# Kernel tuning notes

Measured on AMD Instinct MI355X. Metric: run time of the kernel, lower is better.

## Reference

```python
import jax, jax.numpy as jnp
import numpy as np
from jax import lax

VOCAB, EMBED, HID, B, T = 100, 50, 30, 512, 512
PAD_ID = 0


def setup_inputs() -> dict:
    key = jax.random.key(0)
    ks = jax.random.split(key, 16)
    s_e = 1.0 / np.sqrt(HID)  # torch LSTM/Linear uniform(-1/sqrt(H), 1/sqrt(H)) style
    def u(k, shape, s):
        return jax.random.uniform(k, shape, jnp.float32, -s, s)
    batch_x = jax.random.randint(ks[0], (B, T), 0, VOCAB)
    lens = jax.random.randint(ks[1], (B,), 1, T + 1)
    lens = lens.at[0].set(T)  # ensure pad_packed max length == T
    embedding = jax.random.normal(ks[2], (VOCAB, EMBED), jnp.float32)
    embedding = embedding.at[PAD_ID].set(0.0)  # padding_idx row
    return {
        "batch_x": batch_x,
        "batch_x_lens": lens,
        "embedding": embedding,
        "w_ih1": u(ks[3], (4 * HID, EMBED), s_e),
        "w_hh1": u(ks[4], (4 * HID, HID), s_e),
        "b_ih1": u(ks[5], (4 * HID,), s_e),
        "b_hh1": u(ks[6], (4 * HID,), s_e),
        "w_ih2": u(ks[7], (4 * HID, HID), s_e),
        "w_hh2": u(ks[8], (4 * HID, HID), s_e),
        "b_ih2": u(ks[9], (4 * HID,), s_e),
        "b_hh2": u(ks[10], (4 * HID,), s_e),
        "lw1": u(ks[11], (HID, HID), s_e),
        "lb1": u(ks[12], (HID,), s_e),
        "lw2": u(ks[13], (VOCAB, HID), s_e),
        "lb2": u(ks[14], (VOCAB,), s_e),
    }


def _lstm(x_tbe, mask_tb, w_ih, w_hh, b_ih, b_hh):
    """Masked LSTM over time; state frozen where mask==0 (packed-sequence semantics).
    x_tbe: [T,B,E]; mask_tb: [T,B] bool. Returns hidden seq [T,B,H]."""
    H = w_hh.shape[1]
    Bn = x_tbe.shape[1]
    # precompute input projections for all timesteps (one big GEMM)
    xp = jnp.einsum("tbe,ge->tbg", x_tbe, w_ih) + b_ih + b_hh  # [T,B,4H]

    def step(carry, inp):
        h, c = carry
        xt, mt = inp
        gates = xt + h @ w_hh.T
        i, f, g, o = jnp.split(gates, 4, axis=-1)  # torch gate order i,f,g,o
        i = jax.nn.sigmoid(i)
        f = jax.nn.sigmoid(f)
        g = jnp.tanh(g)
        o = jax.nn.sigmoid(o)
        c_new = f * c + i * g
        h_new = o * jnp.tanh(c_new)
        m = mt[:, None]
        h = jnp.where(m, h_new, h)
        c = jnp.where(m, c_new, c)
        return (h, c), h

    init = (jnp.zeros((Bn, H), x_tbe.dtype), jnp.zeros((Bn, H), x_tbe.dtype))
    _, hs = lax.scan(step, init, (xp, mask_tb))
    return hs


def reference(batch_x, batch_x_lens, embedding,
              w_ih1, w_hh1, b_ih1, b_hh1,
              w_ih2, w_hh2, b_ih2, b_hh2,
              lw1, lb1, lw2, lb2):
    Bn, Tn = batch_x.shape
    mask = (jnp.arange(Tn)[None, :] < batch_x_lens[:, None])  # [B,T]
    x = embedding[batch_x]                                     # [B,T,E]
    x = jnp.transpose(x, (1, 0, 2))                            # [T,B,E]
    m_tb = mask.T                                              # [T,B]
    h1 = _lstm(x, m_tb, w_ih1, w_hh1, b_ih1, b_hh1)            # [T,B,H]
    h2 = _lstm(h1, m_tb, w_ih2, w_hh2, b_ih2, b_hh2)           # [T,B,H]
    out = jnp.transpose(h2, (1, 0, 2))                         # [B,T,H]
    out = jnp.where(mask[:, :, None], out, 0.0)                # pad_packed zero-fill
    hmid = jax.nn.relu(out @ lw1.T + lb1)
    return hmid @ lw2.T + lb2                                  # [B,T,vocab]
```

## Files before the change

kernel.cpp:

```cpp
#include <hip/hip_runtime.h>
#include <math.h>

#define VOCABN 100
#define EMBEDN 50
#define HID 30
#define NB 512
#define NT 512
#define G4 120
#define S 16
#define RD 32

#define L2E 1.44269504089f
#define L2E2 2.88539008178f

__device__ __forceinline__ float fastrcp(float x) {
  float r;
  asm("v_rcp_f32 %0, %1" : "=v"(r) : "v"(x));
  return r;
}
__device__ __forceinline__ float fexp2(float x) {
  float r;
  asm("v_exp_f32 %0, %1" : "=v"(r) : "v"(x));
  return r;
}
__device__ __forceinline__ void bcast_halves(float x, float& lo_all, float& hi_all) {
  auto r = __builtin_amdgcn_permlane32_swap(__builtin_bit_cast(unsigned, x),
                                            __builtin_bit_cast(unsigned, x), false, false);
  lo_all = __builtin_bit_cast(float, (unsigned)r[0]);
  hi_all = __builtin_bit_cast(float, (unsigned)r[1]);
}
__device__ __forceinline__ float rdlane(float v, int k) {
  return __builtin_bit_cast(float, __builtin_amdgcn_readlane(__builtin_bit_cast(int, v), k));
}
__device__ __forceinline__ void tick_barrier() {
  asm volatile("s_waitcnt lgkmcnt(0)" ::: "memory");
  __builtin_amdgcn_s_barrier();
  asm volatile("" ::: "memory");
}

__global__ void prep_kernel(const float* __restrict__ emb,
                            const float* __restrict__ w_ih1,
                            const float* __restrict__ b_ih1,
                            const float* __restrict__ b_hh1,
                            const float* __restrict__ b_ih2,
                            const float* __restrict__ b_hh2,
                            const float* __restrict__ lw2,
                            const float* __restrict__ lb1,
                            const float* __restrict__ lb2,
                            float* __restrict__ xpe, float* __restrict__ b2s,
                            float* __restrict__ outc) {
  __shared__ float e[EMBEDN];
  int r = blockIdx.x;
  int tid = threadIdx.x;
  if (tid < EMBEDN) e[tid] = emb[r * EMBEDN + tid];
  __syncthreads();
  if (tid < G4) {
    float s = b_ih1[tid] + b_hh1[tid];
#pragma unroll
    for (int k = 0; k < EMBEDN; ++k) s = fmaf(e[k], w_ih1[tid * EMBEDN + k], s);
    float sc = (tid >= 2 * HID && tid < 3 * HID) ? L2E2 : L2E;
    xpe[r * G4 + tid] = s * sc;
    if (r == 0) b2s[tid] = (b_ih2[tid] + b_hh2[tid]) * sc;
  }
  if (r == 0 && tid < VOCABN) {
    float o = lb2[tid];
#pragma unroll
    for (int k = 0; k < HID; ++k) o = fmaf(fmaxf(lb1[k], 0.f), lw2[tid * HID + k], o);
    outc[tid] = o;
  }
}

__global__ void __launch_bounds__(256) scan_kernel(
    const int* __restrict__ batch_x, const int* __restrict__ lens,
    const float* __restrict__ xpe, const float* __restrict__ b2s,
    const float* __restrict__ w_hh1, const float* __restrict__ w_ih2,
    const float* __restrict__ w_hh2,
    const float* __restrict__ lw1, const float* __restrict__ lb1,
    const float* __restrict__ lw2, const float* __restrict__ lb2,
    const float* __restrict__ outc, float* __restrict__ out) {
  __shared__ __align__(16) float h1ring[RD][32];
  __shared__ __align__(16) float2 uring[RD][64];
  __shared__ __align__(16) float h2ring[RD][32];
  __shared__ int tok_lds[NT];

  const int b = blockIdx.x;
  const int tid = threadIdx.x;
  const int wid = tid >> 6;
  const int lane = tid & 63;
  const int half = lane >> 5;
  const int j = lane & 31;
  const int jj = (j < HID) ? j : (HID - 1);
  const int gA = half ? (jj + 2 * HID) : jj;
  const int gB = gA + HID;

  const int* xrow = batch_x + b * NT;
  for (int i = tid; i < NT; i += 256) tok_lds[i] = xrow[i];

  const int len = lens[b];
  const int K = (len + S - 1) / S;
  __syncthreads();

  if (wid < 3) {
    const float C1 = half ? 1.0f : L2E2;
    const float C2 = half ? 2.0f : L2E2;
    const float scA = half ? L2E2 : L2E;
    const float* wsrc = (wid == 0) ? w_hh1 : (wid == 1) ? w_ih2 : w_hh2;
    float wA[HID], wB[HID];
#pragma unroll
    for (int k = 0; k < HID; ++k) {
      wA[k] = wsrc[gA * HID + k] * scA;
      wB[k] = wsrc[gB * HID + k] * L2E;
    }
    const float b2A = b2s[gA], b2B = b2s[gB];

    if (wid == 0) {
      float cs1 = 0.f;
      float hs1[HID];
#pragma unroll
      for (int k = 0; k < HID; ++k) hs1[k] = 0.f;
      int tk = tok_lds[0];
      float xa0 = xpe[tk * G4 + gA], xb0 = xpe[tk * G4 + gB];
      tk = tok_lds[1];
      float xa1 = xpe[tk * G4 + gA], xb1 = xpe[tk * G4 + gB];
      tk = tok_lds[2];
      float xa2 = xpe[tk * G4 + gA], xb2 = xpe[tk * G4 + gB];
      int t = 0;
      for (int k = 0; k < K + 3; ++k) {
        if (k < K) {
          int tend = (k + 1) * S;
          tend = (tend < len) ? tend : len;
          for (; t < tend; ++t) {
            float a0a = 0.f, a0b = 0.f, a1a = 0.f, a1b = 0.f;
#pragma unroll
            for (int p = 0; p < 15; ++p) {
              a0a = fmaf(hs1[p], wA[p], a0a);
              a1a = fmaf(hs1[p], wB[p], a1a);
              a0b = fmaf(hs1[p + 15], wA[p + 15], a0b);
              a1b = fmaf(hs1[p + 15], wB[p + 15], a1b);
            }
            float a0 = a0a + a0b + xa0;
            float a1 = a1a + a1b + xb0;
            float sA = C1 - C2 * fastrcp(1.0f + fexp2(a0));
            float sB = 1.0f - fastrcp(1.0f + fexp2(a1));
            float iL, g1, f1, o1;
            bcast_halves(sA, iL, g1);
            bcast_halves(sB, f1, o1);
            cs1 = fmaf(f1, cs1, iL * g1);
            float rr = fastrcp(1.0f + fexp2(cs1));
            float h1n = fmaf(-2.0f * o1, rr, o1);
            if (lane < 32) h1ring[t & (RD - 1)][j] = h1n;
#pragma unroll
            for (int q = 0; q < HID; ++q) hs1[q] = rdlane(h1n, q);
            xa0 = xa1; xb0 = xb1;
            xa1 = xa2; xb1 = xb2;
            int tn = t + 3;
            tk = tok_lds[(tn < NT) ? tn : (NT - 1)];
            xa2 = xpe[tk * G4 + gA];
            xb2 = xpe[tk * G4 + gB];
          }
        }
        tick_barrier();
      }
    } else if (wid == 1) {
      int t = 0;
      for (int k = 0; k < K + 3; ++k) {
        if (k >= 1 && k <= K) {
          int tend = k * S;
          tend = (tend < len) ? tend : len;
          for (; t < tend; ++t) {
            const float2* hp = (const float2*)h1ring[t & (RD - 1)];
            float2 hv[15];
#pragma unroll
            for (int p = 0; p < 15; ++p) hv[p] = hp[p];
            float q0a = 0.f, q0b = 0.f, q1a = 0.f, q1b = 0.f;
#pragma unroll
            for (int p = 0; p < 15; ++p) {
              if (p < 8) {
                q0a = fmaf(hv[p].x, wA[2 * p], q0a);
                q1a = fmaf(hv[p].x, wB[2 * p], q1a);
                q0a = fmaf(hv[p].y, wA[2 * p + 1], q0a);
                q1a = fmaf(hv[p].y, wB[2 * p + 1], q1a);
              } else {
                q0b = fmaf(hv[p].x, wA[2 * p], q0b);
                q1b = fmaf(hv[p].x, wB[2 * p], q1b);
                q0b = fmaf(hv[p].y, wA[2 * p + 1], q0b);
                q1b = fmaf(hv[p].y, wB[2 * p + 1], q1b);
              }
            }
            float2 u;
            u.x = q0a + q0b;
            u.y = q1a + q1b;
            uring[t & (RD - 1)][lane] = u;
          }
        }
        tick_barrier();
      }
    } else {
      float cs2 = 0.f;
      float hs2[HID];
#pragma unroll
      for (int k = 0; k < HID; ++k) hs2[k] = 0.f;
      int t = 0;
      for (int k = 0; k < K + 3; ++k) {
        if (k >= 2) {
          int tend = (k - 1) * S;
          tend = (tend < len) ? tend : len;
          for (; t < tend; ++t) {
            float2 u = uring[t & (RD - 1)][lane];
            float q0a = 0.f, q0b = 0.f, q1a = 0.f, q1b = 0.f;
#pragma unroll
            for (int p = 0; p < 15; ++p) {
              q0a = fmaf(hs2[p], wA[p], q0a);
              q1a = fmaf(hs2[p], wB[p], q1a);
              q0b = fmaf(hs2[p + 15], wA[p + 15], q0b);
              q1b = fmaf(hs2[p + 15], wB[p + 15], q1b);
            }
            float q0 = q0a + q0b + u.x + b2A;
            float q1 = q1a + q1b + u.y + b2B;
            float sA = C1 - C2 * fastrcp(1.0f + fexp2(q0));
            float sB = 1.0f - fastrcp(1.0f + fexp2(q1));
            float iL, g2, f2, o2;
            bcast_halves(sA, iL, g2);
            bcast_halves(sB, f2, o2);
            cs2 = fmaf(f2, cs2, iL * g2);
            float rr = fastrcp(1.0f + fexp2(cs2));
            float h2n = fmaf(-2.0f * o2, rr, o2);
            if (lane < 32) h2ring[t & (RD - 1)][j] = h2n;
#pragma unroll
            for (int q = 0; q < HID; ++q) hs2[q] = rdlane(h2n, q);
          }
        }
        tick_barrier();
      }
    }
  } else {
    const int l1 = (lane < 50) ? lane : 49;
    float w1x[15], w1y[15];
#pragma unroll
    for (int p = 0; p < 15; ++p) {
      w1x[p] = lw1[jj * HID + 2 * p];
      w1y[p] = lw1[jj * HID + 2 * p + 1];
    }
    float w2a[HID], w2b[HID];
#pragma unroll
    for (int k = 0; k < HID; ++k) {
      w2a[k] = lw2[l1 * HID + k];
      w2b[k] = lw2[(l1 + 50) * HID + k];
    }
    const float lb1v = lb1[jj];
    const float lb2a = lb2[l1], lb2b = lb2[l1 + 50];
    const float oca = outc[l1], ocb = outc[l1 + 50];

    int t = 0;
    for (int k = 0; k < K + 3; ++k) {
      if (k >= 3) {
        int tend = (k - 2) * S;
        tend = (tend < len) ? tend : len;
        for (; t < tend; ++t) {
          const float2* hp = (const float2*)h2ring[t & (RD - 1)];
          float2 h[15];
#pragma unroll
          for (int p = 0; p < 15; ++p) h[p] = hp[p];
          float ma = lb1v, mb = 0.f;
#pragma unroll
          for (int p = 0; p < 15; ++p) {
            if (p < 8) {
              ma = fmaf(h[p].x, w1x[p], ma);
              ma = fmaf(h[p].y, w1y[p], ma);
            } else {
              mb = fmaf(h[p].x, w1x[p], mb);
              mb = fmaf(h[p].y, w1y[p], mb);
            }
          }
          float m = fmaxf(ma + mb, 0.f);
          float sm[HID];
#pragma unroll
          for (int q = 0; q < HID; ++q) sm[q] = rdlane(m, q);
          float oa0 = lb2a, oa1 = 0.f, ob0 = lb2b, ob1 = 0.f;
#pragma unroll
          for (int q = 0; q < 15; ++q) {
            oa0 = fmaf(sm[q], w2a[q], oa0);
            ob0 = fmaf(sm[q], w2b[q], ob0);
            oa1 = fmaf(sm[q + 15], w2a[q + 15], oa1);
            ob1 = fmaf(sm[q + 15], w2b[q + 15], ob1);
          }
          float* orow = out + ((size_t)(b * NT + t)) * VOCABN;
          if (lane < 50) {
            orow[l1] = oa0 + oa1;
            orow[l1 + 50] = ob0 + ob1;
          }
        }
      }
      tick_barrier();
    }
    for (int tt = len; tt < NT; ++tt) {
      float* orow = out + ((size_t)(b * NT + tt)) * VOCABN;
      if (lane < 50) {
        orow[l1] = oca;
        orow[l1 + 50] = ocb;
      }
    }
  }
}

extern "C" void kernel_launch(void* const* d_in, const int* in_sizes, int n_in,
                              void* d_out, int out_size, void* d_ws, size_t ws_size,
                              hipStream_t stream) {
  const int* batch_x = (const int*)d_in[0];
  const int* lens = (const int*)d_in[1];
  const float* emb = (const float*)d_in[2];
  const float* w_ih1 = (const float*)d_in[3];
  const float* w_hh1 = (const float*)d_in[4];
  const float* b_ih1 = (const float*)d_in[5];
  const float* b_hh1 = (const float*)d_in[6];
  const float* w_ih2 = (const float*)d_in[7];
  const float* w_hh2 = (const float*)d_in[8];
  const float* b_ih2 = (const float*)d_in[9];
  const float* b_hh2 = (const float*)d_in[10];
  const float* lw1 = (const float*)d_in[11];
  const float* lb1 = (const float*)d_in[12];
  const float* lw2 = (const float*)d_in[13];
  const float* lb2 = (const float*)d_in[14];
  float* out = (float*)d_out;

  char* ws = (char*)d_ws;
  float* xpe = (float*)ws;
  float* b2s = (float*)(ws + 48 * 1024);
  float* outc = (float*)(ws + 56 * 1024);

  prep_kernel<<<VOCABN, 128, 0, stream>>>(emb, w_ih1, b_ih1, b_hh1, b_ih2, b_hh2,
                                          lw2, lb1, lb2, xpe, b2s, outc);
  scan_kernel<<<NB, 256, 0, stream>>>(batch_x, lens, xpe, b2s, w_hh1, w_ih2, w_hh2,
                                      lw1, lb1, lw2, lb2, outc, out);
}
```

Before: 268.9 us.

## Use packed fp16 dot2 for recurrent matvecs and compute all four gates per lane

The recurrent h@W_hh products in both LSTM layers now use fp16-packed weights and hidden state with v_dot2 accumulation into fp32. Each lane computes all four gates for its hidden unit, so the permlane32 half-swap broadcast is no longer needed. The change targets the latency of the serial per-timestep critical path by halving the FMA count and removing the cross-half exchange. In exchange it adds fp16 rounding (round-toward-zero) to weights and hidden state, which can cause accuracy drift over 512 recurrent steps, and it shortens the input-projection prefetch depth from three steps to two.

```diff
diff --git a/kernel.cpp b/kernel.cpp
--- a/kernel.cpp
+++ b/kernel.cpp
@@ -13,6 +13,8 @@
 #define L2E 1.44269504089f
 #define L2E2 2.88539008178f
 
+typedef __fp16 h2v __attribute__((ext_vector_type(2)));
+
 __device__ __forceinline__ float fastrcp(float x) {
   float r;
   asm("v_rcp_f32 %0, %1" : "=v"(r) : "v"(x));
@@ -22,12 +24,6 @@
   float r;
   asm("v_exp_f32 %0, %1" : "=v"(r) : "v"(x));
   return r;
-}
-__device__ __forceinline__ void bcast_halves(float x, float& lo_all, float& hi_all) {
-  auto r = __builtin_amdgcn_permlane32_swap(__builtin_bit_cast(unsigned, x),
-                                            __builtin_bit_cast(unsigned, x), false, false);
-  lo_all = __builtin_bit_cast(float, (unsigned)r[0]);
-  hi_all = __builtin_bit_cast(float, (unsigned)r[1]);
 }
 __device__ __forceinline__ float rdlane(float v, int k) {
   return __builtin_bit_cast(float, __builtin_amdgcn_readlane(__builtin_bit_cast(int, v), k));
@@ -70,6 +66,32 @@
   }
 }
 
+#define DOT4(ai, af, ag, ao, HP, W0_, W1_, W2_, W3_, I0, I1, I2, I3)  \
+  float ai = (I0), af = (I1), ag = (I2), ao = (I3);                   \
+  float ai1 = 0.f, af1 = 0.f, ag1 = 0.f, ao1 = 0.f;                   \
+  _Pragma("unroll") for (int p = 0; p < 8; ++p) {                     \
+    ai = __builtin_amdgcn_fdot2(HP[p], W0_[p], ai, false);            \
+    af = __builtin_amdgcn_fdot2(HP[p], W1_[p], af, false);            \
+    ag = __builtin_amdgcn_fdot2(HP[p], W2_[p], ag, false);            \
+    ao = __builtin_amdgcn_fdot2(HP[p], W3_[p], ao, false);            \
+  }                                                                   \
+  _Pragma("unroll") for (int p = 8; p < 15; ++p) {                    \
+    ai1 = __builtin_amdgcn_fdot2(HP[p], W0_[p], ai1, false);          \
+    af1 = __builtin_amdgcn_fdot2(HP[p], W1_[p], af1, false);          \
+    ag1 = __builtin_amdgcn_fdot2(HP[p], W2_[p], ag1, false);          \
+    ao1 = __builtin_amdgcn_fdot2(HP[p], W3_[p], ao1, false);          \
+  }                                                                   \
+  ai += ai1; af += af1; ag += ag1; ao += ao1;
+
+#define NONLIN_H(ai, af, ag, ao, cs, hout)                 \
+  float iS = L2E2 - L2E2 * fastrcp(1.0f + fexp2(ai));      \
+  float f_ = 1.0f - fastrcp(1.0f + fexp2(af));             \
+  float g_ = 1.0f - 2.0f * fastrcp(1.0f + fexp2(ag));      \
+  float o_ = 1.0f - fastrcp(1.0f + fexp2(ao));             \
+  cs = fmaf(f_, cs, iS * g_);                              \
+  float rr = fastrcp(1.0f + fexp2(cs));                    \
+  float hout = fmaf(-2.0f * o_, rr, o_);
+
 __global__ void __launch_bounds__(256) scan_kernel(
     const int* __restrict__ batch_x, const int* __restrict__ lens,
     const float* __restrict__ xpe, const float* __restrict__ b2s,
@@ -90,8 +112,6 @@
   const int half = lane >> 5;
   const int j = lane & 31;
   const int jj = (j < HID) ? j : (HID - 1);
-  const int gA = half ? (jj + 2 * HID) : jj;
-  const int gB = gA + HID;
 
   const int* xrow = batch_x + b * NT;
   for (int i = tid; i < NT; i += 256) tok_lds[i] = xrow[i];
@@ -100,138 +120,122 @@
   const int K = (len + S - 1) / S;
   __syncthreads();
 
-  if (wid < 3) {
-    const float C1 = half ? 1.0f : L2E2;
-    const float C2 = half ? 2.0f : L2E2;
-    const float scA = half ? L2E2 : L2E;
-    const float* wsrc = (wid == 0) ? w_hh1 : (wid == 1) ? w_ih2 : w_hh2;
-    float wA[HID], wB[HID];
-#pragma unroll
-    for (int k = 0; k < HID; ++k) {
-      wA[k] = wsrc[gA * HID + k] * scA;
-      wB[k] = wsrc[gB * HID + k] * L2E;
-    }
-    const float b2A = b2s[gA], b2B = b2s[gB];
+  if (wid == 0 || wid == 2) {
+    const float* wsrc = (wid == 0) ? w_hh1 : w_hh2;
+    h2v wfi[15], wff[15], wfg[15], wfo[15];
+#pragma unroll
+    for (int p = 0; p < 15; ++p) {
+      const float* ri = wsrc + (0 * HID + jj) * HID;
+      const float* rf = wsrc + (1 * HID + jj) * HID;
+      const float* rg = wsrc + (2 * HID + jj) * HID;
+      const float* ro = wsrc + (3 * HID + jj) * HID;
+      wfi[p] = __builtin_amdgcn_cvt_pkrtz(ri[2 * p] * L2E, ri[2 * p + 1] * L2E);
+      wff[p] = __builtin_amdgcn_cvt_pkrtz(rf[2 * p] * L2E, rf[2 * p + 1] * L2E);
+      wfg[p] = __builtin_amdgcn_cvt_pkrtz(rg[2 * p] * L2E2, rg[2 * p + 1] * L2E2);
+      wfo[p] = __builtin_amdgcn_cvt_pkrtz(ro[2 * p] * L2E, ro[2 * p + 1] * L2E);
+    }
+    h2v hp[15];
+#pragma unroll
+    for (int p = 0; p < 15; ++p) hp[p] = h2v{(__fp16)0.0f, (__fp16)0.0f};
+    float cs = 0.f;
 
     if (wid == 0) {
-      float cs1 = 0.f;
-      float hs1[HID];
-#pragma unroll
-      for (int k = 0; k < HID; ++k) hs1[k] = 0.f;
       int tk = tok_lds[0];
-      float xa0 = xpe[tk * G4 + gA], xb0 = xpe[tk * G4 + gB];
+      float x0i = xpe[tk * G4 + jj], x0f = xpe[tk * G4 + HID + jj];
+      float x0g = xpe[tk * G4 + 2 * HID + jj], x0o = xpe[tk * G4 + 3 * HID + jj];
       tk = tok_lds[1];
-      float xa1 = xpe[tk * G4 + gA], xb1 = xpe[tk * G4 + gB];
-      tk = tok_lds[2];
-      float xa2 = xpe[tk * G4 + gA], xb2 = xpe[tk * G4 + gB];
+      float x1i = xpe[tk * G4 + jj], x1f = xpe[tk * G4 + HID + jj];
+      float x1g = xpe[tk * G4 + 2 * HID + jj], x1o = xpe[tk * G4 + 3 * HID + jj];
       int t = 0;
       for (int k = 0; k < K + 3; ++k) {
         if (k < K) {
           int tend = (k + 1) * S;
           tend = (tend < len) ? tend : len;
           for (; t < tend; ++t) {
-            float a0a = 0.f, a0b = 0.f, a1a = 0.f, a1b = 0.f;
-#pragma unroll
-            for (int p = 0; p < 15; ++p) {
-              a0a = fmaf(hs1[p], wA[p], a0a);
-              a1a = fmaf(hs1[p], wB[p], a1a);
-              a0b = fmaf(hs1[p + 15], wA[p + 15], a0b);
-              a1b = fmaf(hs1[p + 15], wB[p + 15], a1b);
-            }
-            float a0 = a0a + a0b + xa0;
-            float a1 = a1a + a1b + xb0;
-            float sA = C1 - C2 * fastrcp(1.0f + fexp2(a0));
-            float sB = 1.0f - fastrcp(1.0f + fexp2(a1));
-            float iL, g1, f1, o1;
-            bcast_halves(sA, iL, g1);
-            bcast_halves(sB, f1, o1);
-            cs1 = fmaf(f1, cs1, iL * g1);
-            float rr = fastrcp(1.0f + fexp2(cs1));
-            float h1n = fmaf(-2.0f * o1, rr, o1);
+            DOT4(ai, af, ag, ao, hp, wfi, wff, wfg, wfo, x0i, x0f, x0g, x0o)
+            NONLIN_H(ai, af, ag, ao, cs, h1n)
             if (lane < 32) h1ring[t & (RD - 1)][j] = h1n;
 #pragma unroll
-            for (int q = 0; q < HID; ++q) hs1[q] = rdlane(h1n, q);
-            xa0 = xa1; xb0 = xb1;
-            xa1 = xa2; xb1 = xb2;
-            int tn = t + 3;
+            for (int q = 0; q < 15; ++q)
+              hp[q] = __builtin_amdgcn_cvt_pkrtz(rdlane(h1n, 2 * q),
+                                                 rdlane(h1n, 2 * q + 1));
+            x0i = x1i; x0f = x1f; x0g = x1g; x0o = x1o;
+            int tn = t + 2;
             tk = tok_lds[(tn < NT) ? tn : (NT - 1)];
-            xa2 = xpe[tk * G4 + gA];
-            xb2 = xpe[tk * G4 + gB];
+            x1i = xpe[tk * G4 + jj];
+            x1f = xpe[tk * G4 + HID + jj];
+            x1g = xpe[tk * G4 + 2 * HID + jj];
+            x1o = xpe[tk * G4 + 3 * HID + jj];
           }
         }
         tick_barrier();
       }
-    } else if (wid == 1) {
-      int t = 0;
-      for (int k = 0; k < K + 3; ++k) {
-        if (k >= 1 && k <= K) {
-          int tend = k * S;
-          tend = (tend < len) ? tend : len;
-          for (; t < tend; ++t) {
-            const float2* hp = (const float2*)h1ring[t & (RD - 1)];
-            float2 hv[15];
-#pragma unroll
-            for (int p = 0; p < 15; ++p) hv[p] = hp[p];
-            float q0a = 0.f, q0b = 0.f, q1a = 0.f, q1b = 0.f;
-#pragma unroll
-            for (int p = 0; p < 15; ++p) {
-              if (p < 8) {
-                q0a = fmaf(hv[p].x, wA[2 * p], q0a);
-                q1a = fmaf(hv[p].x, wB[2 * p], q1a);
-                q0a = fmaf(hv[p].y, wA[2 * p + 1], q0a);
-                q1a = fmaf(hv[p].y, wB[2 * p + 1], q1a);
-              } else {
-                q0b = fmaf(hv[p].x, wA[2 * p], q0b);
-                q1b = fmaf(hv[p].x, wB[2 * p], q1b);
-                q0b = fmaf(hv[p].y, wA[2 * p + 1], q0b);
-                q1b = fmaf(hv[p].y, wB[2 * p + 1], q1b);
-              }
-            }
-            float2 u;
-            u.x = q0a + q0b;
-            u.y = q1a + q1b;
-            uring[t & (RD - 1)][lane] = u;
-          }
-        }
-        tick_barrier();
-      }
     } else {
-      float cs2 = 0.f;
-      float hs2[HID];
-#pragma unroll
-      for (int k = 0; k < HID; ++k) hs2[k] = 0.f;
+      const float b2i = b2s[jj], b2f = b2s[HID + jj];
+      const float b2g = b2s[2 * HID + jj], b2o = b2s[3 * HID + jj];
       int t = 0;
       for (int k = 0; k < K + 3; ++k) {
         if (k >= 2) {
           int tend = (k - 1) * S;
           tend = (tend < len) ? tend : len;
           for (; t < tend; ++t) {
-            float2 u = uring[t & (RD - 1)][lane];
-            float q0a = 0.f, q0b = 0.f, q1a = 0.f, q1b = 0.f;
-#pragma unroll
-            for (int p = 0; p < 15; ++p) {
-              q0a = fmaf(hs2[p], wA[p], q0a);
-              q1a = fmaf(hs2[p], wB[p], q1a);
-              q0b = fmaf(hs2[p + 15], wA[p + 15], q0b);
-              q1b = fmaf(hs2[p + 15], wB[p + 15], q1b);
-            }
-            float q0 = q0a + q0b + u.x + b2A;
-            float q1 = q1a + q1b + u.y + b2B;
-            float sA = C1 - C2 * fastrcp(1.0f + fexp2(q0));
-            float sB = 1.0f - fastrcp(1.0f + fexp2(q1));
-            float iL, g2, f2, o2;
-            bcast_halves(sA, iL, g2);
-            bcast_halves(sB, f2, o2);
-            cs2 = fmaf(f2, cs2, iL * g2);
-            float rr = fastrcp(1.0f + fexp2(cs2));
-            float h2n = fmaf(-2.0f * o2, rr, o2);
+            float2 uif = uring[t & (RD - 1)][jj];
+            float2 ugo = uring[t & (RD - 1)][jj + 32];
+            DOT4(ai, af, ag, ao, hp, wfi, wff, wfg, wfo,
+                 uif.x + b2i, uif.y + b2f, ugo.x + b2g, ugo.y + b2o)
+            NONLIN_H(ai, af, ag, ao, cs, h2n)
             if (lane < 32) h2ring[t & (RD - 1)][j] = h2n;
 #pragma unroll
-            for (int q = 0; q < HID; ++q) hs2[q] = rdlane(h2n, q);
+            for (int q = 0; q < 15; ++q)
+              hp[q] = __builtin_amdgcn_cvt_pkrtz(rdlane(h2n, 2 * q),
+                                                 rdlane(h2n, 2 * q + 1));
           }
         }
         tick_barrier();
       }
+    }
+  } else if (wid == 1) {
+    const int gA = half ? (jj + 2 * HID) : jj;
+    const int gB = gA + HID;
+    const float scA = half ? L2E2 : L2E;
+    float wA[HID], wB[HID];
+#pragma unroll
+    for (int k = 0; k < HID; ++k) {
+      wA[k] = w_ih2[gA * HID + k] * scA;
+      wB[k] = w_ih2[gB * HID + k] * L2E;
+    }
+    int t = 0;
+    for (int k = 0; k < K + 3; ++k) {
+      if (k >= 1 && k <= K) {
+        int tend = k * S;
+        tend = (tend < len) ? tend : len;
+        for (; t < tend; ++t) {
+          const float2* hpd = (const float2*)h1ring[t & (RD - 1)];
+          float2 hv[15];
+#pragma unroll
+          for (int p = 0; p < 15; ++p) hv[p] = hpd[p];
+          float q0a = 0.f, q0b = 0.f, q1a = 0.f, q1b = 0.f;
+#pragma unroll
+          for (int p = 0; p < 15; ++p) {
+            if (p < 8) {
+              q0a = fmaf(hv[p].x, wA[2 * p], q0a);
+              q1a = fmaf(hv[p].x, wB[2 * p], q1a);
+              q0a = fmaf(hv[p].y, wA[2 * p + 1], q0a);
+              q1a = fmaf(hv[p].y, wB[2 * p + 1], q1a);
+            } else {
+              q0b = fmaf(hv[p].x, wA[2 * p], q0b);
+              q1b = fmaf(hv[p].x, wB[2 * p], q1b);
+              q0b = fmaf(hv[p].y, wA[2 * p + 1], q0b);
+              q1b = fmaf(hv[p].y, wB[2 * p + 1], q1b);
+            }
+          }
+          float2 u;
+          u.x = q0a + q0b;
+          u.y = q1a + q1b;
+          uring[t & (RD - 1)][lane] = u;
+        }
+      }
+      tick_barrier();
     }
   } else {
     const int l1 = (lane < 50) ? lane : 49;
@@ -257,10 +261,10 @@
         int tend = (k - 2) * S;
         tend = (tend < len) ? tend : len;
         for (; t < tend; ++t) {
-          const float2* hp = (const float2*)h2ring[t & (RD - 1)];
+          const float2* hpd = (const float2*)h2ring[t & (RD - 1)];
           float2 h[15];
 #pragma unroll
-          for (int p = 0; p < 15; ++p) h[p] = hp[p];
+          for (int p = 0; p < 15; ++p) h[p] = hpd[p];
           float ma = lb1v, mb = 0.f;
 #pragma unroll
           for (int p = 0; p < 15; ++p) {
```

Measured after the change: 330.2 us. 22.8% more time.
